# Kernel tuning notes

Measured on AMD Instinct MI355X. Metric: run time of the kernel, lower is better.

The kernel has to match this reference:

```python
import jax, jax.numpy as jnp
import numpy as np

B_, D_, L_, N_ = 2, 1536, 2048, 16


def setup_inputs() -> dict:
    key = jax.random.key(0)
    ks = jax.random.split(key, 8)
    x = jax.random.normal(ks[0], (B_, D_, L_), dtype=jnp.float32)
    delta = jax.random.normal(ks[1], (B_, D_, L_), dtype=jnp.float32)
    # A negative (as in Mamba, A = -exp(A_log)) so the recurrence is stable
    A = -(jax.random.uniform(ks[2], (D_, N_), dtype=jnp.float32) + 0.5)
    B = jax.random.normal(ks[3], (B_, N_, L_), dtype=jnp.float32)
    C = jax.random.normal(ks[4], (B_, N_, L_), dtype=jnp.float32)
    D = jax.random.normal(ks[5], (D_,), dtype=jnp.float32)
    z = jax.random.normal(ks[6], (B_, D_, L_), dtype=jnp.float32)
    delta_bias = jax.random.normal(ks[7], (D_,), dtype=jnp.float32)
    return {"x": x, "delta": delta, "A": A, "B": B, "C": C,
            "D": D, "z": z, "delta_bias": delta_bias}


def reference(x, delta, A, B, C, D, z, delta_bias):
    # delta_softplus=True path with delta_bias, variable B (bnl) and C (bnl)
    delta = jax.nn.softplus(delta + delta_bias[None, :, None])      # (b,d,l)
    deltaA = jnp.exp(jnp.einsum('bdl,dn->bdln', delta, A))          # (b,d,l,n)
    deltaB_x = jnp.einsum('bdl,bnl,bdl->bdln', delta, B, x)         # (b,d,l,n)

    # scan over the sequence axis: h = deltaA_t * h + deltaB_x_t; y = h @ C_t
    dA_t = jnp.transpose(deltaA, (2, 0, 1, 3))     # (l,b,d,n)
    dBx_t = jnp.transpose(deltaB_x, (2, 0, 1, 3))  # (l,b,d,n)
    C_t = jnp.transpose(C, (2, 0, 1))              # (l,b,n)

    def step(h, inp):
        dA_i, dBx_i, C_i = inp
        h = dA_i * h + dBx_i                       # (b,d,n)
        y = jnp.einsum('bdn,bn->bd', h, C_i)       # (b,d)
        return h, y

    h0 = jnp.zeros((x.shape[0], A.shape[0], A.shape[1]), dtype=jnp.float32)
    _, ys = jax.lax.scan(step, h0, (dA_t, dBx_t, C_t))  # ys: (l,b,d)
    y = jnp.transpose(ys, (1, 2, 0))                    # (b,d,l)

    out = y + x * D[None, :, None]                      # D skip connection
    out = out * (z * jax.nn.sigmoid(z))                 # SiLU gate
    return out
```

## Files before the change

kernel.cpp:

```cpp
#include <hip/hip_runtime.h>
#include <math.h>

#define B_  2
#define D_  1536
#define L_  2048
#define N_  16
#define NH  8
#define LC  128
#define NCHUNK (L_ / LC)
#define NCH (B_ * D_)
#define LOG2E 1.4426950408889634f
#define LN2   0.6931471805599453f

typedef float f4 __attribute__((ext_vector_type(4)));
typedef float f8 __attribute__((ext_vector_type(8)));

__device__ __forceinline__ float exp2f_(float v) { return __builtin_amdgcn_exp2f(v); }
__device__ __forceinline__ float log2f_(float v) { return __builtin_amdgcn_logf(v); }
__device__ __forceinline__ float rcpf_(float v)  { return __builtin_amdgcn_rcpf(v); }

__device__ __forceinline__ float softplus_f(float v) {
    float t = exp2f_(v * LOG2E);
    float r = LN2 * log2f_(1.0f + t);
    return (v > 20.0f) ? v : r;
}
__device__ __forceinline__ f8 splat8(float v) { f8 r = {v,v,v,v,v,v,v,v}; return r; }
__device__ __forceinline__ f8 exp2v8(f8 a) {
    f8 r;
    r[0]=exp2f_(a[0]); r[1]=exp2f_(a[1]); r[2]=exp2f_(a[2]); r[3]=exp2f_(a[3]);
    r[4]=exp2f_(a[4]); r[5]=exp2f_(a[5]); r[6]=exp2f_(a[6]); r[7]=exp2f_(a[7]);
    return r;
}
__device__ __forceinline__ float dot8(f8 a, f8 b) {
    float p0 = fmaf(a[0], b[0], a[1]*b[1]);
    float p1 = fmaf(a[2], b[2], a[3]*b[3]);
    float p2 = fmaf(a[4], b[4], a[5]*b[5]);
    float p3 = fmaf(a[6], b[6], a[7]*b[7]);
    return (p0 + p1) + (p2 + p3);
}

__global__ __launch_bounds__(64, 3)
void ssm_scan_kernel(const float* __restrict__ x,
                     const float* __restrict__ delta,
                     const float* __restrict__ A,
                     const float* __restrict__ Bm,
                     const float* __restrict__ Cm,
                     const float* __restrict__ Dv,
                     const float* __restrict__ z,
                     const float* __restrict__ dbias,
                     float* __restrict__ out)
{
    const int lane = threadIdx.x;
    const int s    = lane & 31;
    const int g    = lane >> 5;
    const int ch   = blockIdx.x;
    const int b    = ch / D_;
    const int d    = ch - b * D_;

    const float bias = dbias[d];
    const float Dd   = Dv[d];

    const float* Ab = A + d * N_ + NH * g;
    f8 A2v;
    A2v[0]=Ab[0]*LOG2E; A2v[1]=Ab[1]*LOG2E; A2v[2]=Ab[2]*LOG2E; A2v[3]=Ab[3]*LOG2E;
    A2v[4]=Ab[4]*LOG2E; A2v[5]=Ab[5]*LOG2E; A2v[6]=Ab[6]*LOG2E; A2v[7]=Ab[7]*LOG2E;

    const float* Bp = Bm + (size_t)b * (N_ * L_) + (size_t)(NH * g) * L_;
    const float* Cp = Cm + (size_t)b * (N_ * L_) + (size_t)(NH * g) * L_;
    const size_t chbase = (size_t)ch * L_;

    f8 carry = splat8(0.0f);

    for (int c = 0; c < NCHUNK; ++c) {
        const int off = c * LC + s * 4;

        f4 dv = *(const f4*)(delta + chbase + off);
        f4 xv = *(const f4*)(x     + chbase + off);
        f4 zv = *(const f4*)(z     + chbase + off);
#define LD_BC(i) f4 Bv##i = *(const f4*)(Bp + i * L_ + off); \
                 f4 Cv##i = *(const f4*)(Cp + i * L_ + off);
        LD_BC(0) LD_BC(1) LD_BC(2) LD_BC(3) LD_BC(4) LD_BC(5) LD_BC(6) LD_BC(7)

        float dt0 = softplus_f(dv.x + bias);
        float dt1 = softplus_f(dv.y + bias);
        float dt2 = softplus_f(dv.z + bias);
        float dt3 = softplus_f(dv.w + bias);
        float u0 = dt0 * xv.x, u1 = dt1 * xv.y, u2 = dt2 * xv.z, u3 = dt3 * xv.w;
        float dtsum = (dt0 + dt1) + (dt2 + dt3);

        f8 e0 = exp2v8(splat8(dt0) * A2v);
        f8 e1 = exp2v8(splat8(dt1) * A2v);
        f8 e2 = exp2v8(splat8(dt2) * A2v);
        f8 e3 = exp2v8(splat8(dt3) * A2v);
        f8 P  = exp2v8(splat8(dtsum) * A2v);

        f8 tB0 = {Bv0.x,Bv1.x,Bv2.x,Bv3.x,Bv4.x,Bv5.x,Bv6.x,Bv7.x};
        f8 tB1 = {Bv0.y,Bv1.y,Bv2.y,Bv3.y,Bv4.y,Bv5.y,Bv6.y,Bv7.y};
        f8 tB2 = {Bv0.z,Bv1.z,Bv2.z,Bv3.z,Bv4.z,Bv5.z,Bv6.z,Bv7.z};
        f8 tB3 = {Bv0.w,Bv1.w,Bv2.w,Bv3.w,Bv4.w,Bv5.w,Bv6.w,Bv7.w};
        f8 uB0 = splat8(u0) * tB0;
        f8 uB1 = splat8(u1) * tB1;
        f8 uB2 = splat8(u2) * tB2;
        f8 uB3 = splat8(u3) * tB3;
        f8 SC0 = {Cv0.x,Cv1.x,Cv2.x,Cv3.x,Cv4.x,Cv5.x,Cv6.x,Cv7.x};
        f8 SC1 = {Cv0.y,Cv1.y,Cv2.y,Cv3.y,Cv4.y,Cv5.y,Cv6.y,Cv7.y};
        f8 SC2 = {Cv0.z,Cv1.z,Cv2.z,Cv3.z,Cv4.z,Cv5.z,Cv6.z,Cv7.z};
        f8 SC3 = {Cv0.w,Cv1.w,Cv2.w,Cv3.w,Cv4.w,Cv5.w,Cv6.w,Cv7.w};

        f8 S = uB0;
        S = e1 * S + uB1;
        S = e2 * S + uB2;
        S = e3 * S + uB3;

#pragma unroll
        for (int o = 1; o < 32; o <<= 1) {
#define SCANI(i) { float Pp = __shfl_up(P[i], o, 32); \
                   float Sp = __shfl_up(S[i], o, 32); \
                   Pp = (s >= o) ? Pp : 1.0f; \
                   Sp = (s >= o) ? Sp : 0.0f; \
                   S[i] = fmaf(Sp, P[i], S[i]); \
                   P[i] = P[i] * Pp; }
            SCANI(0) SCANI(1) SCANI(2) SCANI(3) SCANI(4) SCANI(5) SCANI(6) SCANI(7)
        }

        f8 h;
#define CARRYI(i) { float hinc = fmaf(carry[i], P[i], S[i]); \
                    float hup  = __shfl_up(hinc, 1, 32); \
                    h[i] = (s == 0) ? carry[i] : hup; \
                    carry[i] = __shfl(hinc, 31, 32); }
        CARRYI(0) CARRYI(1) CARRYI(2) CARRYI(3) CARRYI(4) CARRYI(5) CARRYI(6) CARRYI(7)

        h = e0 * h + uB0;  float y0 = dot8(h, SC0);
        h = e1 * h + uB1;  float y1 = dot8(h, SC1);
        h = e2 * h + uB2;  float y2 = dot8(h, SC2);
        h = e3 * h + uB3;  float y3 = dot8(h, SC3);

        y0 += __shfl_xor(y0, 32, 64);
        y1 += __shfl_xor(y1, 32, 64);
        y2 += __shfl_xor(y2, 32, 64);
        y3 += __shfl_xor(y3, 32, 64);
        if (g == 0) {
            float s0 = rcpf_(1.0f + exp2f_(-zv.x * LOG2E));
            float s1 = rcpf_(1.0f + exp2f_(-zv.y * LOG2E));
            float s2 = rcpf_(1.0f + exp2f_(-zv.z * LOG2E));
            float s3 = rcpf_(1.0f + exp2f_(-zv.w * LOG2E));
            f4 ov = { (y0 + xv.x * Dd) * (zv.x * s0),
                      (y1 + xv.y * Dd) * (zv.y * s1),
                      (y2 + xv.z * Dd) * (zv.z * s2),
                      (y3 + xv.w * Dd) * (zv.w * s3) };
            *(f4*)(out + chbase + off) = ov;
        }
    }
}

extern "C" void kernel_launch(void* const* d_in, const int* in_sizes, int n_in,
                              void* d_out, int out_size, void* d_ws, size_t ws_size,
                              hipStream_t stream) {
    const float* x     = (const float*)d_in[0];
    const float* delta = (const float*)d_in[1];
    const float* A     = (const float*)d_in[2];
    const float* Bm    = (const float*)d_in[3];
    const float* Cm    = (const float*)d_in[4];
    const float* Dv    = (const float*)d_in[5];
    const float* z     = (const float*)d_in[6];
    const float* dbias = (const float*)d_in[7];
    float* out = (float*)d_out;

    dim3 grid(NCH);
    dim3 block(64);
    ssm_scan_kernel<<<grid, block, 0, stream>>>(x, delta, A, Bm, Cm, Dv, z, dbias, out);
}
```

Baseline: 179.7 us.

## Repartition scan: 4 state groups of 4, 8 timesteps per lane

Changes the wave's work split from 2 groups of 8 states with 4 timesteps per lane to 4 groups of 4 states with 8 timesteps per lane. The cross-lane scan shrinks to 16 lanes with half as many state elements, cutting shuffle count, and the B/C transposes disappear since each lane now holds contiguous timesteps. The cost is longer sequential per-lane recurrences and an extra xor-shuffle level in the output reduction. Sigmoid and output math now run on all lanes even though only one group stores.

```diff
diff --git a/kernel.cpp b/kernel.cpp
--- a/kernel.cpp
+++ b/kernel.cpp
@@ -5,7 +5,6 @@
 #define D_  1536
 #define L_  2048
 #define N_  16
-#define NH  8
 #define LC  128
 #define NCHUNK (L_ / LC)
 #define NCH (B_ * D_)
@@ -19,11 +18,6 @@
 __device__ __forceinline__ float log2f_(float v) { return __builtin_amdgcn_logf(v); }
 __device__ __forceinline__ float rcpf_(float v)  { return __builtin_amdgcn_rcpf(v); }
 
-__device__ __forceinline__ float softplus_f(float v) {
-    float t = exp2f_(v * LOG2E);
-    float r = LN2 * log2f_(1.0f + t);
-    return (v > 20.0f) ? v : r;
-}
 __device__ __forceinline__ f8 splat8(float v) { f8 r = {v,v,v,v,v,v,v,v}; return r; }
 __device__ __forceinline__ f8 exp2v8(f8 a) {
     f8 r;
@@ -31,12 +25,15 @@
     r[4]=exp2f_(a[4]); r[5]=exp2f_(a[5]); r[6]=exp2f_(a[6]); r[7]=exp2f_(a[7]);
     return r;
 }
-__device__ __forceinline__ float dot8(f8 a, f8 b) {
-    float p0 = fmaf(a[0], b[0], a[1]*b[1]);
-    float p1 = fmaf(a[2], b[2], a[3]*b[3]);
-    float p2 = fmaf(a[4], b[4], a[5]*b[5]);
-    float p3 = fmaf(a[6], b[6], a[7]*b[7]);
-    return (p0 + p1) + (p2 + p3);
+__device__ __forceinline__ f8 softplus8(f8 v) {
+    f8 r;
+#pragma unroll
+    for (int j = 0; j < 8; ++j) {
+        float t = exp2f_(v[j] * LOG2E);
+        float u = LN2 * log2f_(1.0f + t);
+        r[j] = (v[j] > 20.0f) ? v[j] : u;
+    }
+    return r;
 }
 
 __global__ __launch_bounds__(64, 3)
@@ -51,8 +48,8 @@
                      float* __restrict__ out)
 {
     const int lane = threadIdx.x;
-    const int s    = lane & 31;
-    const int g    = lane >> 5;
+    const int s    = lane & 15;
+    const int g    = lane >> 4;
     const int ch   = blockIdx.x;
     const int b    = ch / D_;
     const int d    = ch - b * D_;
@@ -60,95 +57,102 @@
     const float bias = dbias[d];
     const float Dd   = Dv[d];
 
-    const float* Ab = A + d * N_ + NH * g;
-    f8 A2v;
-    A2v[0]=Ab[0]*LOG2E; A2v[1]=Ab[1]*LOG2E; A2v[2]=Ab[2]*LOG2E; A2v[3]=Ab[3]*LOG2E;
-    A2v[4]=Ab[4]*LOG2E; A2v[5]=Ab[5]*LOG2E; A2v[6]=Ab[6]*LOG2E; A2v[7]=Ab[7]*LOG2E;
+    const float* Ab = A + d * N_ + 4 * g;
+    f4 A2 = { Ab[0]*LOG2E, Ab[1]*LOG2E, Ab[2]*LOG2E, Ab[3]*LOG2E };
 
-    const float* Bp = Bm + (size_t)b * (N_ * L_) + (size_t)(NH * g) * L_;
-    const float* Cp = Cm + (size_t)b * (N_ * L_) + (size_t)(NH * g) * L_;
+    const float* Bp = Bm + (size_t)b * (N_ * L_) + (size_t)(4 * g) * L_;
+    const float* Cp = Cm + (size_t)b * (N_ * L_) + (size_t)(4 * g) * L_;
     const size_t chbase = (size_t)ch * L_;
 
-    f8 carry = splat8(0.0f);
+    f4 carry = {0.0f, 0.0f, 0.0f, 0.0f};
 
     for (int c = 0; c < NCHUNK; ++c) {
-        const int off = c * LC + s * 4;
+        const int off = c * LC + s * 8;
 
-        f4 dv = *(const f4*)(delta + chbase + off);
-        f4 xv = *(const f4*)(x     + chbase + off);
-        f4 zv = *(const f4*)(z     + chbase + off);
-#define LD_BC(i) f4 Bv##i = *(const f4*)(Bp + i * L_ + off); \
-                 f4 Cv##i = *(const f4*)(Cp + i * L_ + off);
-        LD_BC(0) LD_BC(1) LD_BC(2) LD_BC(3) LD_BC(4) LD_BC(5) LD_BC(6) LD_BC(7)
+        f8 dv = *(const f8*)(delta + chbase + off);
+        f8 xv = *(const f8*)(x     + chbase + off);
+        f8 zv = *(const f8*)(z     + chbase + off);
+        f8 Bv0 = *(const f8*)(Bp + 0 * L_ + off);
+        f8 Bv1 = *(const f8*)(Bp + 1 * L_ + off);
+        f8 Bv2 = *(const f8*)(Bp + 2 * L_ + off);
+        f8 Bv3 = *(const f8*)(Bp + 3 * L_ + off);
+        f8 Cv0 = *(const f8*)(Cp + 0 * L_ + off);
+        f8 Cv1 = *(const f8*)(Cp + 1 * L_ + off);
+        f8 Cv2 = *(const f8*)(Cp + 2 * L_ + off);
+        f8 Cv3 = *(const f8*)(Cp + 3 * L_ + off);
 
-        float dt0 = softplus_f(dv.x + bias);
-        float dt1 = softplus_f(dv.y + bias);
-        float dt2 = softplus_f(dv.z + bias);
-        float dt3 = softplus_f(dv.w + bias);
-        float u0 = dt0 * xv.x, u1 = dt1 * xv.y, u2 = dt2 * xv.z, u3 = dt3 * xv.w;
-        float dtsum = (dt0 + dt1) + (dt2 + dt3);
+        f8 dt = softplus8(dv + splat8(bias));
+        f8 u  = dt * xv;
+        float dtsum = ((dt[0]+dt[1]) + (dt[2]+dt[3])) + ((dt[4]+dt[5]) + (dt[6]+dt[7]));
 
-        f8 e0 = exp2v8(splat8(dt0) * A2v);
-        f8 e1 = exp2v8(splat8(dt1) * A2v);
-        f8 e2 = exp2v8(splat8(dt2) * A2v);
-        f8 e3 = exp2v8(splat8(dt3) * A2v);
-        f8 P  = exp2v8(splat8(dtsum) * A2v);
+        f8 e0 = exp2v8(dt * splat8(A2[0]));
+        f8 e1 = exp2v8(dt * splat8(A2[1]));
+        f8 e2 = exp2v8(dt * splat8(A2[2]));
+        f8 e3 = exp2v8(dt * splat8(A2[3]));
+        f4 P = { exp2f_(dtsum * A2[0]), exp2f_(dtsum * A2[1]),
+                 exp2f_(dtsum * A2[2]), exp2f_(dtsum * A2[3]) };
 
-        f8 tB0 = {Bv0.x,Bv1.x,Bv2.x,Bv3.x,Bv4.x,Bv5.x,Bv6.x,Bv7.x};
-        f8 tB1 = {Bv0.y,Bv1.y,Bv2.y,Bv3.y,Bv4.y,Bv5.y,Bv6.y,Bv7.y};
-        f8 tB2 = {Bv0.z,Bv1.z,Bv2.z,Bv3.z,Bv4.z,Bv5.z,Bv6.z,Bv7.z};
-        f8 tB3 = {Bv0.w,Bv1.w,Bv2.w,Bv3.w,Bv4.w,Bv5.w,Bv6.w,Bv7.w};
-        f8 uB0 = splat8(u0) * tB0;
-        f8 uB1 = splat8(u1) * tB1;
-        f8 uB2 = splat8(u2) * tB2;
-        f8 uB3 = splat8(u3) * tB3;
-        f8 SC0 = {Cv0.x,Cv1.x,Cv2.x,Cv3.x,Cv4.x,Cv5.x,Cv6.x,Cv7.x};
-        f8 SC1 = {Cv0.y,Cv1.y,Cv2.y,Cv3.y,Cv4.y,Cv5.y,Cv6.y,Cv7.y};
-        f8 SC2 = {Cv0.z,Cv1.z,Cv2.z,Cv3.z,Cv4.z,Cv5.z,Cv6.z,Cv7.z};
-        f8 SC3 = {Cv0.w,Cv1.w,Cv2.w,Cv3.w,Cv4.w,Cv5.w,Cv6.w,Cv7.w};
+        f8 uB0 = u * Bv0;
+        f8 uB1 = u * Bv1;
+        f8 uB2 = u * Bv2;
+        f8 uB3 = u * Bv3;
 
-        f8 S = uB0;
-        S = e1 * S + uB1;
-        S = e2 * S + uB2;
-        S = e3 * S + uB3;
+        f4 S;
+#define LOCAL_SCAN(i) { float acc = uB##i[0]; \
+        acc = fmaf(e##i[1], acc, uB##i[1]); \
+        acc = fmaf(e##i[2], acc, uB##i[2]); \
+        acc = fmaf(e##i[3], acc, uB##i[3]); \
+        acc = fmaf(e##i[4], acc, uB##i[4]); \
+        acc = fmaf(e##i[5], acc, uB##i[5]); \
+        acc = fmaf(e##i[6], acc, uB##i[6]); \
+        acc = fmaf(e##i[7], acc, uB##i[7]); \
+        S[i] = acc; }
+        LOCAL_SCAN(0) LOCAL_SCAN(1) LOCAL_SCAN(2) LOCAL_SCAN(3)
 
 #pragma unroll
-        for (int o = 1; o < 32; o <<= 1) {
-#define SCANI(i) { float Pp = __shfl_up(P[i], o, 32); \
-                   float Sp = __shfl_up(S[i], o, 32); \
+        for (int o = 1; o < 16; o <<= 1) {
+#define SCANI(i) { float Pp = __shfl_up(P[i], o, 16); \
+                   float Sp = __shfl_up(S[i], o, 16); \
                    Pp = (s >= o) ? Pp : 1.0f; \
                    Sp = (s >= o) ? Sp : 0.0f; \
                    S[i] = fmaf(Sp, P[i], S[i]); \
                    P[i] = P[i] * Pp; }
-            SCANI(0) SCANI(1) SCANI(2) SCANI(3) SCANI(4) SCANI(5) SCANI(6) SCANI(7)
+            SCANI(0) SCANI(1) SCANI(2) SCANI(3)
         }
 
-        f8 h;
+        f4 h;
 #define CARRYI(i) { float hinc = fmaf(carry[i], P[i], S[i]); \
-                    float hup  = __shfl_up(hinc, 1, 32); \
+                    float hup  = __shfl_up(hinc, 1, 16); \
                     h[i] = (s == 0) ? carry[i] : hup; \
-                    carry[i] = __shfl(hinc, 31, 32); }
-        CARRYI(0) CARRYI(1) CARRYI(2) CARRYI(3) CARRYI(4) CARRYI(5) CARRYI(6) CARRYI(7)
+                    carry[i] = __shfl(hinc, 15, 16); }
+        CARRYI(0) CARRYI(1) CARRYI(2) CARRYI(3)
 
-        h = e0 * h + uB0;  float y0 = dot8(h, SC0);
-        h = e1 * h + uB1;  float y1 = dot8(h, SC1);
-        h = e2 * h + uB2;  float y2 = dot8(h, SC2);
-        h = e3 * h + uB3;  float y3 = dot8(h, SC3);
+        f8 y = splat8(0.0f);
+#define PASS2(i) { float hi = h[i]; \
+        hi = fmaf(e##i[0], hi, uB##i[0]); y[0] = fmaf(hi, Cv##i[0], y[0]); \
+        hi = fmaf(e##i[1], hi, uB##i[1]); y[1] = fmaf(hi, Cv##i[1], y[1]); \
+        hi = fmaf(e##i[2], hi, uB##i[2]); y[2] = fmaf(hi, Cv##i[2], y[2]); \
+        hi = fmaf(e##i[3], hi, uB##i[3]); y[3] = fmaf(hi, Cv##i[3], y[3]); \
+        hi = fmaf(e##i[4], hi, uB##i[4]); y[4] = fmaf(hi, Cv##i[4], y[4]); \
+        hi = fmaf(e##i[5], hi, uB##i[5]); y[5] = fmaf(hi, Cv##i[5], y[5]); \
+        hi = fmaf(e##i[6], hi, uB##i[6]); y[6] = fmaf(hi, Cv##i[6], y[6]); \
+        hi = fmaf(e##i[7], hi, uB##i[7]); y[7] = fmaf(hi, Cv##i[7], y[7]); }
+        PASS2(0) PASS2(1) PASS2(2) PASS2(3)
 
-        y0 += __shfl_xor(y0, 32, 64);
-        y1 += __shfl_xor(y1, 32, 64);
-        y2 += __shfl_xor(y2, 32, 64);
-        y3 += __shfl_xor(y3, 32, 64);
+#pragma unroll
+        for (int j = 0; j < 8; ++j) {
+            y[j] += __shfl_xor(y[j], 16, 64);
+            y[j] += __shfl_xor(y[j], 32, 64);
+        }
+
+        f8 ov;
+#pragma unroll
+        for (int j = 0; j < 8; ++j) {
+            float sig = rcpf_(1.0f + exp2f_(-zv[j] * LOG2E));
+            ov[j] = (y[j] + xv[j] * Dd) * (zv[j] * sig);
+        }
         if (g == 0) {
-            float s0 = rcpf_(1.0f + exp2f_(-zv.x * LOG2E));
-            float s1 = rcpf_(1.0f + exp2f_(-zv.y * LOG2E));
-            float s2 = rcpf_(1.0f + exp2f_(-zv.z * LOG2E));
-            float s3 = rcpf_(1.0f + exp2f_(-zv.w * LOG2E));
-            f4 ov = { (y0 + xv.x * Dd) * (zv.x * s0),
-                      (y1 + xv.y * Dd) * (zv.y * s1),
-                      (y2 + xv.z * Dd) * (zv.z * s2),
-                      (y3 + xv.w * Dd) * (zv.w * s3) };
-            *(f4*)(out + chbase + off) = ov;
+            *(f8*)(out + chbase + off) = ov;
         }
     }
 }
```

After: 194.4 us. 1.08x slower.
